# Kernel optimization log

Measured on AMD Instinct MI355X. Metric: run time of the kernel, lower is better.

## Reference

```python
import jax, jax.numpy as jnp
import numpy as np

N_EMBED = 16384
EMBED_DIM = 256
BETA = 1.0  # default forward arg


def setup_inputs() -> dict:
    key = jax.random.key(0)
    k1, k2 = jax.random.split(key)
    z = jax.random.normal(k1, (8, EMBED_DIM, 32, 32), dtype=jnp.float32)
    # nn.Embedding init: uniform(-1/n_embed, 1/n_embed)
    embed_w = jax.random.uniform(k2, (N_EMBED, EMBED_DIM), dtype=jnp.float32,
                                 minval=-1.0 / N_EMBED, maxval=1.0 / N_EMBED)
    return {"z": z, "embed_w": embed_w}


def reference(z, embed_w):
    B, C, H, W = z.shape
    zb = jnp.transpose(z, (0, 2, 3, 1))            # (B,H,W,C)
    zf = zb.reshape(B * H * W, C)                  # (BHW, C)
    # squared L2 distances to every code: ||z||^2 + ||e||^2 - 2 z.e
    d = (jnp.sum(zf ** 2, axis=1, keepdims=True)
         + jnp.sum(embed_w ** 2, axis=1)
         - 2.0 * jnp.einsum('bd,nd->bn', zf, embed_w))  # (BHW, n_embed)
    idx = jnp.argmin(d, axis=1)                    # (BHW,)
    z_q = embed_w[idx].reshape(B, H, W, C)         # codebook gather
    loss = (BETA * jnp.mean((jax.lax.stop_gradient(z_q) - zb) ** 2)
            + jnp.mean((z_q - jax.lax.stop_gradient(zb)) ** 2))
    # straight-through estimator
    z_q = zb + jax.lax.stop_gradient(z_q - zb)
    z_q = jnp.transpose(z_q, (0, 3, 1, 2))         # (B,C,H,W)
    return z_q, loss
```

## Files before the change

### kernel.cpp

```cpp
#include <hip/hip_runtime.h>
#include <hip/hip_bf16.h>
#include <stdint.h>


typedef __attribute__((ext_vector_type(8))) short bf16x8;
typedef __attribute__((ext_vector_type(8))) unsigned short ushort8v;
typedef __attribute__((ext_vector_type(4))) float f32x4;

__device__ __forceinline__ unsigned short f2bf(float f) {
  unsigned u = __float_as_uint(f);
  return (unsigned short)((u + 0x7FFFu + ((u >> 16) & 1u)) >> 16);
}

typedef const __attribute__((address_space(1))) unsigned char* gas1;
typedef __attribute__((address_space(3))) unsigned char* las3;
__device__ __forceinline__ void cp16g(const void* g, void* l) {
  __builtin_amdgcn_global_load_lds((gas1)g, (las3)l, 16, 0, 0);
}

__global__ void k_prep(const float* __restrict__ z, const float* __restrict__ ew,
                       unsigned short* __restrict__ zp, unsigned short* __restrict__ ep,
                       float* __restrict__ h2, float* __restrict__ out) {
  __shared__ unsigned char smem[16896];
  int bid = blockIdx.x;
  int t = threadIdx.x;
  if (bid < 512) {
    float (*tile)[132] = (float (*)[132])smem;
    int b = bid >> 6, ct = (bid >> 3) & 7, hwt = bid & 7;
    const float* src = z + b * 262144 + ct * 32768 + hwt * 128;
#pragma unroll
    for (int it = 0; it < 4; ++it) {
      int cell = it * 1024 + t * 4;
      int cl = cell >> 7, hl = cell & 127;
      float4 v = *(const float4*)(src + cl * 1024 + hl);
      *(float4*)(&tile[cl][hl]) = v;
    }
    __syncthreads();
    int mt = b * 8 + hwt;
    unsigned short* dst = zp + mt * 32768 + ct * 4096;
#pragma unroll
    for (int it = 0; it < 2; ++it) {
      int cell = it * 256 + t;
      int kg = cell >> 7, r = cell & 127;
      ushort8v v;
#pragma unroll
      for (int j = 0; j < 8; ++j) v[j] = f2bf(tile[kg * 8 + j][r]);
      *(ushort8v*)(dst + cell * 8) = v;
    }
  } else {
    unsigned short (*et)[264] = (unsigned short (*)[264])smem;
    if (bid == 512 && t == 0) out[2097152] = 0.0f;
    int n0 = (bid - 512) * 32;
    int lane = t & 63;
#pragma unroll
    for (int it = 0; it < 4; ++it) {
      int c = it * 8 + (t >> 5);
      int k0 = (t & 31) * 8;
      const float4 x = *(const float4*)(ew + (n0 + c) * 256 + k0);
      const float4 y = *(const float4*)(ew + (n0 + c) * 256 + k0 + 4);
      float s = x.x * x.x + x.y * x.y + x.z * x.z + x.w * x.w
              + y.x * y.x + y.y * y.y + y.z * y.z + y.w * y.w;
      ushort8v v;
      v[0] = f2bf(x.x); v[1] = f2bf(x.y); v[2] = f2bf(x.z); v[3] = f2bf(x.w);
      v[4] = f2bf(y.x); v[5] = f2bf(y.y); v[6] = f2bf(y.z); v[7] = f2bf(y.w);
      *(ushort8v*)(&et[c][k0]) = v;
#pragma unroll
      for (int off = 1; off <= 16; off <<= 1) s += __shfl_xor(s, off);
      if ((lane & 31) == 0) h2[n0 + c] = -0.5f * s;
    }
    __syncthreads();
    int nb = n0 >> 7, col0 = n0 & 127;
#pragma unroll
    for (int it = 0; it < 4; ++it) {
      int cellk = it * 8 + (t >> 5);
      int c = t & 31;
      int ks = cellk >> 2, kg = cellk & 3;
      ushort8v v = *(const ushort8v*)(&et[c][cellk * 8]);
      *(ushort8v*)(ep + nb * 32768 + ks * 4096 + kg * 1024 + (col0 + c) * 8) = v;
    }
  }
}

__global__ __launch_bounds__(256, 3) void k_main(
    const unsigned short* __restrict__ zp, const unsigned short* __restrict__ ep,
    const float* __restrict__ h2, int2* __restrict__ partial) {
  __shared__ unsigned char ring[49152];
  __shared__ float hbuf[1024];
  int seg = blockIdx.x;
  int mt = blockIdx.y;
  int t = threadIdx.x, wv = t >> 6, lane = t & 63;
  int l15 = lane & 15, kg = lane >> 4;

  bf16x8 av[16];
  const unsigned short* abase = zp + mt * 32768;
#pragma unroll
  for (int m = 0; m < 2; ++m)
#pragma unroll
    for (int ks = 0; ks < 8; ++ks)
      av[m * 8 + ks] = *(const bf16x8*)(abase + ks * 4096 + kg * 1024 +
                                        (wv * 32 + m * 16 + l15) * 8);

  const unsigned char* bsrc = (const unsigned char*)ep + seg * 524288;
  const unsigned char* bstage = bsrc + wv * 1024 + lane * 16;
  int ldsw = wv * 1024;

  cp16g((const unsigned char*)(h2 + seg * 1024) + ldsw + lane * 16,
        (unsigned char*)hbuf + ldsw);
#pragma unroll
  for (int i = 0; i < 4; ++i)
    cp16g(bstage + i * 4096, &ring[i * 4096 + ldsw]);
  __builtin_amdgcn_sched_barrier(0);
#pragma unroll
  for (int i = 0; i < 4; ++i)
    cp16g(bstage + 16384 + i * 4096, &ring[16384 + i * 4096 + ldsw]);

  f32x4 acc[2][8];
  float best[2][4];
#pragma unroll
  for (int m = 0; m < 2; ++m)
#pragma unroll
    for (int r = 0; r < 4; ++r) best[m][r] = -3.4e38f;

  unsigned rd = 0u, wr = 32768u;

#define KSTEP(PH, NB, DOSTAGE, VM)                                              \
  {                                                                             \
    asm volatile("s_waitcnt vmcnt(" VM ")" ::: "memory");                       \
    __builtin_amdgcn_s_barrier();                                               \
    if (DOSTAGE) {                                                              \
      const unsigned char* sg = bstage + ((NB) * 4 + (PH) + 2) * 16384;         \
      _Pragma("unroll") for (int i = 0; i < 4; ++i)                             \
        cp16g(sg + i * 4096, &ring[wr + i * 4096 + ldsw]);                      \
    }                                                                           \
    if ((PH) == 0) {                                                            \
      _Pragma("unroll") for (int nf = 0; nf < 8; ++nf)                          \
        acc[0][nf] = acc[1][nf] = (f32x4){0.f, 0.f, 0.f, 0.f};                  \
    }                                                                           \
    __builtin_amdgcn_s_setprio(1);                                              \
    _Pragma("unroll") for (int k2 = 0; k2 < 2; ++k2) {                          \
      bf16x8 bv[8];                                                             \
      _Pragma("unroll") for (int nf = 0; nf < 8; ++nf)                          \
        bv[nf] = *(const bf16x8*)(&ring[rd + k2 * 8192 + kg * 2048 +            \
                                        (nf * 16 + l15) * 16]);                 \
      _Pragma("unroll") for (int m = 0; m < 2; ++m)                             \
        _Pragma("unroll") for (int nf = 0; nf < 8; ++nf)                        \
          acc[m][nf] = __builtin_amdgcn_mfma_f32_16x16x32_bf16(                 \
              av[m * 8 + (PH) * 2 + k2], bv[nf], acc[m][nf], 0, 0, 0);          \
    }                                                                           \
    __builtin_amdgcn_s_setprio(0);                                              \
    if ((PH) == 3) {                                                            \
      unsigned colbase = (unsigned)((NB) * 128 + l15);                          \
      _Pragma("unroll") for (int nf = 0; nf < 8; ++nf) {                        \
        float h = hbuf[(NB) * 128 + nf * 16 + l15];                             \
        unsigned lcol = colbase + nf * 16u;                                     \
        _Pragma("unroll") for (int m = 0; m < 2; ++m)                           \
          _Pragma("unroll") for (int r = 0; r < 4; ++r) {                       \
            unsigned p = (__float_as_uint(acc[m][nf][r] + h) & 0xFFFFF800u) | lcol; \
            best[m][r] = fmaxf(best[m][r], __uint_as_float(p));                 \
          }                                                                     \
      }                                                                         \
    }                                                                           \
    rd = (rd == 32768u) ? 0u : rd + 16384u;                                     \
    wr = (wr == 32768u) ? 0u : wr + 16384u;                                     \
  }

#pragma unroll 1
  for (int nb = 0; nb < 7; ++nb) {
    KSTEP(0, nb, 1, "4")
    KSTEP(1, nb, 1, "4")
    KSTEP(2, nb, 1, "4")
    KSTEP(3, nb, 1, "4")
  }
  KSTEP(0, 7, 1, "4")
  KSTEP(1, 7, 1, "4")
  KSTEP(2, 7, 0, "4")
  KSTEP(3, 7, 0, "0")
#undef KSTEP

#pragma unroll
  for (int m = 0; m < 2; ++m)
#pragma unroll
    for (int r = 0; r < 4; ++r) {
      float bvv = best[m][r];
#pragma unroll
      for (int off = 1; off <= 8; off <<= 1) bvv = fmaxf(bvv, __shfl_xor(bvv, off));
      if (l15 == 0) {
        unsigned bits = __float_as_uint(bvv);
        int gidx = seg * 1024 + (int)(bits & 0x7FFu);
        int row = mt * 128 + wv * 32 + m * 16 + kg * 4 + r;
        partial[seg * 8192 + row] = make_int2((int)bits, gidx);
      }
    }
}

__global__ void k_fin(const int2* __restrict__ partial, const float* __restrict__ ew,
                      const float* __restrict__ z, float* __restrict__ out) {
  __shared__ float tile[32][260];
  __shared__ int codeIdx[32];
  int bid = blockIdx.x;
  int b = bid >> 5, pxt = bid & 31;
  int t = threadIdx.x, wv = t >> 6, lane = t & 63;
  if (t < 32) {
    int row = b * 1024 + pxt * 32 + t;
    float bb = -3.4e38f;
    int bi = 0;
#pragma unroll
    for (int s = 0; s < 16; ++s) {
      int2 p = partial[s * 8192 + row];
      float v = __int_as_float(p.x);
      if (v > bb) { bb = v; bi = p.y; }
    }
    codeIdx[t] = bi;
  }
  __syncthreads();
#pragma unroll
  for (int i = 0; i < 8; ++i) {
    int px = wv * 8 + i;
    int idx = codeIdx[px];
    float4 v = *(const float4*)(ew + idx * 256 + lane * 4);
    *(float4*)(&tile[px][lane * 4]) = v;
  }
  __syncthreads();
  float ls = 0.0f;
  int zbase = b * 262144 + pxt * 32;
#pragma unroll
  for (int j = 0; j < 8; ++j) {
    int c = wv * 64 + j * 8 + (lane >> 3);
    int p4 = (lane & 7) * 4;
    float4 q;
    q.x = tile[p4][c]; q.y = tile[p4 + 1][c]; q.z = tile[p4 + 2][c]; q.w = tile[p4 + 3][c];
    const float* zp_ = z + zbase + c * 1024 + p4;
    float4 zv = *(const float4*)zp_;
    float dx = q.x - zv.x, dy = q.y - zv.y, dz = q.z - zv.z, dw = q.w - zv.w;
    ls += dx * dx + dy * dy + dz * dz + dw * dw;
    *(float4*)(out + zbase + c * 1024 + p4) = q;
  }
#pragma unroll
  for (int off = 32; off; off >>= 1) ls += __shfl_xor(ls, off);
  if (lane == 0) atomicAdd(out + 2097152, ls * (2.0f / 2097152.0f));
}

extern "C" void kernel_launch(void* const* d_in, const int* in_sizes, int n_in,
                              void* d_out, int out_size, void* d_ws, size_t ws_size,
                              hipStream_t stream) {
  const float* z = (const float*)d_in[0];
  const float* ew = (const float*)d_in[1];
  float* out = (float*)d_out;
  unsigned char* ws = (unsigned char*)d_ws;
  unsigned short* zp = (unsigned short*)ws;
  unsigned short* ep = (unsigned short*)(ws + (4u << 20));
  float* h2 = (float*)(ws + (12u << 20));
  int2* partial = (int2*)(ws + (12u << 20) + 65536);

  k_prep<<<1024, 256, 0, stream>>>(z, ew, zp, ep, h2, out);
  k_main<<<dim3(16, 64), 256, 0, stream>>>(zp, ep, h2, partial);
  k_fin<<<256, 256, 0, stream>>>(partial, ew, z, out);
}
```

Baseline: 188.1 us.

## Use 4-slot static LDS ring, fold bias into accumulator init, parallelize final reduction

The main kernel's LDS ring grows from three to four 16KB slots indexed statically by phase, removing the runtime rd/wr pointer rotation. Occupancy hint drops from 3 to 2 blocks per CU to fit the larger buffer. The -0.5||e||^2 bias now initializes the accumulators instead of being added in the argmax epilogue. The finalize kernel reduces the 16 segment partials with 256 threads and shuffles instead of 32 serial threads, and pads the tile to 261 columns to avoid LDS bank conflicts. Lower occupancy may reduce latency hiding.

```diff
diff --git a/kernel.cpp b/kernel.cpp
--- a/kernel.cpp
+++ b/kernel.cpp
@@ -81,10 +81,10 @@
   }
 }
 
-__global__ __launch_bounds__(256, 3) void k_main(
+__global__ __launch_bounds__(256, 2) void k_main(
     const unsigned short* __restrict__ zp, const unsigned short* __restrict__ ep,
     const float* __restrict__ h2, int2* __restrict__ partial) {
-  __shared__ unsigned char ring[49152];
+  __shared__ unsigned char ring[4][16384];
   __shared__ float hbuf[1024];
   int seg = blockIdx.x;
   int mt = blockIdx.y;
@@ -108,11 +108,11 @@
         (unsigned char*)hbuf + ldsw);
 #pragma unroll
   for (int i = 0; i < 4; ++i)
-    cp16g(bstage + i * 4096, &ring[i * 4096 + ldsw]);
+    cp16g(bstage + i * 4096, &ring[0][i * 4096 + ldsw]);
   __builtin_amdgcn_sched_barrier(0);
 #pragma unroll
   for (int i = 0; i < 4; ++i)
-    cp16g(bstage + 16384 + i * 4096, &ring[16384 + i * 4096 + ldsw]);
+    cp16g(bstage + 16384 + i * 4096, &ring[1][i * 4096 + ldsw]);
 
   f32x4 acc[2][8];
   float best[2][4];
@@ -120,8 +120,6 @@
   for (int m = 0; m < 2; ++m)
 #pragma unroll
     for (int r = 0; r < 4; ++r) best[m][r] = -3.4e38f;
-
-  unsigned rd = 0u, wr = 32768u;
 
 #define KSTEP(PH, NB, DOSTAGE, VM)                                              \
   {                                                                             \
@@ -130,18 +128,21 @@
     if (DOSTAGE) {                                                              \
       const unsigned char* sg = bstage + ((NB) * 4 + (PH) + 2) * 16384;         \
       _Pragma("unroll") for (int i = 0; i < 4; ++i)                             \
-        cp16g(sg + i * 4096, &ring[wr + i * 4096 + ldsw]);                      \
+        cp16g(sg + i * 4096, &ring[((PH) + 2) & 3][i * 4096 + ldsw]);           \
     }                                                                           \
     if ((PH) == 0) {                                                            \
-      _Pragma("unroll") for (int nf = 0; nf < 8; ++nf)                          \
-        acc[0][nf] = acc[1][nf] = (f32x4){0.f, 0.f, 0.f, 0.f};                  \
+      _Pragma("unroll") for (int nf = 0; nf < 8; ++nf) {                        \
+        float h = hbuf[(NB) * 128 + nf * 16 + l15];                             \
+        acc[0][nf] = (f32x4){h, h, h, h};                                       \
+        acc[1][nf] = acc[0][nf];                                                \
+      }                                                                         \
     }                                                                           \
     __builtin_amdgcn_s_setprio(1);                                              \
     _Pragma("unroll") for (int k2 = 0; k2 < 2; ++k2) {                          \
       bf16x8 bv[8];                                                             \
       _Pragma("unroll") for (int nf = 0; nf < 8; ++nf)                          \
-        bv[nf] = *(const bf16x8*)(&ring[rd + k2 * 8192 + kg * 2048 +            \
-                                        (nf * 16 + l15) * 16]);                 \
+        bv[nf] = *(const bf16x8*)(&ring[(PH)][k2 * 8192 + kg * 2048 +           \
+                                             (nf * 16 + l15) * 16]);            \
       _Pragma("unroll") for (int m = 0; m < 2; ++m)                             \
         _Pragma("unroll") for (int nf = 0; nf < 8; ++nf)                        \
           acc[m][nf] = __builtin_amdgcn_mfma_f32_16x16x32_bf16(                 \
@@ -150,18 +151,15 @@
     __builtin_amdgcn_s_setprio(0);                                              \
     if ((PH) == 3) {                                                            \
       unsigned colbase = (unsigned)((NB) * 128 + l15);                          \
-      _Pragma("unroll") for (int nf = 0; nf < 8; ++nf) {                        \
-        float h = hbuf[(NB) * 128 + nf * 16 + l15];                             \
-        unsigned lcol = colbase + nf * 16u;                                     \
-        _Pragma("unroll") for (int m = 0; m < 2; ++m)                           \
+      _Pragma("unroll") for (int m = 0; m < 2; ++m)                             \
+        _Pragma("unroll") for (int nf = 0; nf < 8; ++nf) {                      \
+          unsigned lcol = colbase + nf * 16u;                                   \
           _Pragma("unroll") for (int r = 0; r < 4; ++r) {                       \
-            unsigned p = (__float_as_uint(acc[m][nf][r] + h) & 0xFFFFF800u) | lcol; \
+            unsigned p = (__float_as_uint(acc[m][nf][r]) & 0xFFFFF800u) | lcol; \
             best[m][r] = fmaxf(best[m][r], __uint_as_float(p));                 \
           }                                                                     \
-      }                                                                         \
-    }                                                                           \
-    rd = (rd == 32768u) ? 0u : rd + 16384u;                                     \
-    wr = (wr == 32768u) ? 0u : wr + 16384u;                                     \
+        }                                                                       \
+    }                                                                           \
   }
 
 #pragma unroll 1
@@ -195,22 +193,26 @@
 
 __global__ void k_fin(const int2* __restrict__ partial, const float* __restrict__ ew,
                       const float* __restrict__ z, float* __restrict__ out) {
-  __shared__ float tile[32][260];
+  __shared__ float tile[32][261];
   __shared__ int codeIdx[32];
   int bid = blockIdx.x;
   int b = bid >> 5, pxt = bid & 31;
   int t = threadIdx.x, wv = t >> 6, lane = t & 63;
-  if (t < 32) {
-    int row = b * 1024 + pxt * 32 + t;
-    float bb = -3.4e38f;
-    int bi = 0;
-#pragma unroll
-    for (int s = 0; s < 16; ++s) {
-      int2 p = partial[s * 8192 + row];
-      float v = __int_as_float(p.x);
-      if (v > bb) { bb = v; bi = p.y; }
-    }
-    codeIdx[t] = bi;
+#pragma unroll
+  for (int half = 0; half < 2; ++half) {
+    int local = half * 16 + (t >> 4);
+    int segi = t & 15;
+    int row = b * 1024 + pxt * 32 + local;
+    int2 p = partial[segi * 8192 + row];
+    float v = __int_as_float(p.x);
+    int bi = p.y;
+#pragma unroll
+    for (int off = 1; off <= 8; off <<= 1) {
+      float ov = __shfl_xor(v, off);
+      int obi = __shfl_xor(bi, off);
+      if (ov > v) { v = ov; bi = obi; }
+    }
+    if (segi == 0) codeIdx[local] = bi;
   }
   __syncthreads();
 #pragma unroll
```

After: 155.6 us. 1.21x faster.
